# Performance work log

Hardware: AMD Instinct MI355X
Metric: run time of the kernel (lower is better)

The kernel has to match this reference:

```python
import jax, jax.numpy as jnp
import numpy as np

MIN_EXPERT_CAPACITY = 4
EPS = 1e-9
CAPACITY_FACTOR = 1.25  # training-mode capacity factor
LOSS_COEF = 0.01


def _top1(t):
    idx = jnp.argmax(t, axis=-1)
    val = jnp.take_along_axis(t, idx[..., None], axis=-1)[..., 0]
    return val, idx


def _cumsum_exclusive(t):
    # exclusive cumsum along the group (token) axis, dim=-2
    return jnp.cumsum(t, axis=-2) - t


def _top2_gating(logits, importance=None):
    """lucidrains Top2Gating, policy='all', training capacity factor.
    logits: [..., group, num_gates]. Returns (dispatch [...,g,e,c], combine, loss)."""
    group_size = logits.shape[-2]
    num_gates = logits.shape[-1]
    raw_gates = jax.nn.softmax(logits, axis=-1)

    gate_1, index_1 = _top1(raw_gates)
    mask_1 = jax.nn.one_hot(index_1, num_gates, dtype=raw_gates.dtype)
    density_1_proxy = raw_gates
    if importance is not None:
        eq_one = (importance == 1.0).astype(raw_gates.dtype)
        mask_1 = mask_1 * eq_one[..., None]
        gate_1 = gate_1 * eq_one
        density_1_proxy = density_1_proxy * eq_one[..., None]

    gate_2, index_2 = _top1(raw_gates * (1.0 - mask_1))
    mask_2 = jax.nn.one_hot(index_2, num_gates, dtype=raw_gates.dtype)
    if importance is not None:
        mask_2 = mask_2 * (importance > 0.0).astype(raw_gates.dtype)[..., None]

    denom = gate_1 + gate_2 + EPS
    gate_1 = gate_1 / denom
    gate_2 = gate_2 / denom

    density_1 = mask_1.mean(axis=-2)
    loss = jnp.mean(density_1_proxy.mean(axis=-2) * density_1) * (num_gates ** 2)

    # second_policy == 'all': keep every second-place expert
    cap = max(MIN_EXPERT_CAPACITY, min(group_size, int(group_size * CAPACITY_FACTOR / num_gates)))

    pos_1 = _cumsum_exclusive(mask_1) * mask_1
    mask_1 = mask_1 * (pos_1 < cap).astype(mask_1.dtype)
    mask_1_count = mask_1.sum(axis=-2, keepdims=True)
    mask_1_flat = mask_1.sum(axis=-1)
    pos_1 = pos_1.sum(axis=-1)
    gate_1 = gate_1 * mask_1_flat

    pos_2 = (_cumsum_exclusive(mask_2) + mask_1_count) * mask_2
    mask_2 = mask_2 * (pos_2 < cap).astype(mask_2.dtype)
    mask_2_flat = mask_2.sum(axis=-1)
    pos_2 = pos_2.sum(axis=-1)
    gate_2 = gate_2 * mask_2_flat

    combine = (
        gate_1[..., None, None] * mask_1_flat[..., None, None]
        * jax.nn.one_hot(index_1, num_gates, dtype=gate_1.dtype)[..., None]
        * jax.nn.one_hot(pos_1.astype(jnp.int32), cap, dtype=gate_1.dtype)[..., None, :]
        + gate_2[..., None, None] * mask_2_flat[..., None, None]
        * jax.nn.one_hot(index_2, num_gates, dtype=gate_2.dtype)[..., None]
        * jax.nn.one_hot(pos_2.astype(jnp.int32), cap, dtype=gate_2.dtype)[..., None, :]
    )
    dispatch = (combine != 0).astype(combine.dtype)
    return dispatch, combine, loss


def setup_inputs() -> dict:
    B, N, D, EO, EI, H = 8, 2048, 1024, 4, 4, 4096
    k = jax.random.split(jax.random.key(0), 5)
    return {
        "inputs": jax.random.normal(k[0], (B, N, D), jnp.float32),
        "w_gate_outer": jax.random.normal(k[1], (D, EO), jnp.float32) * D ** -0.5,
        "w_gate_inner": jax.random.normal(k[2], (EO, D, EI), jnp.float32) * D ** -0.5,
        "w1": jax.random.uniform(k[3], (EO, EI, D, H), jnp.float32, -(H ** -0.5), H ** -0.5),
        "w2": jax.random.uniform(k[4], (EO, EI, H, D), jnp.float32, -(D ** -0.5), D ** -0.5),
    }


def reference(inputs, w_gate_outer, w_gate_inner, w1, w2):
    # outer gating over tokens: [b,n,d] -> dispatch [b,n,eo,c_o]
    disp_o, comb_o, loss_o = _top2_gating(jnp.einsum('bnd,de->bne', inputs, w_gate_outer))
    exp_in_o = jnp.einsum('bnd,bnec->ebcd', inputs, disp_o)          # [eo,b,c_o,d]

    importance = comb_o.transpose(2, 0, 3, 1).sum(axis=-1)           # [eo,b,c_o]
    importance = 0.5 * ((importance > 0.5).astype(inputs.dtype)
                        + (importance > 0.0).astype(inputs.dtype))

    # inner gating per outer expert: [eo,b,c_o,d] -> dispatch [eo,b,c_o,ei,c_i]
    disp_i, comb_i, loss_i = _top2_gating(
        jnp.einsum('ebnd,edg->ebng', exp_in_o, w_gate_inner), importance=importance)
    exp_in = jnp.einsum('ebnd,ebnfc->efbcd', exp_in_o, disp_i)       # [eo,ei,b,c_i,d]

    # grouped-expert FFN (ReLU)
    hidden = jax.nn.relu(jnp.einsum('efbcd,efdh->efbch', exp_in, w1))
    exp_out = jnp.einsum('efbch,efhd->efbcd', hidden, w2)

    out_o = jnp.einsum('efbcd,ebnfc->ebnd', exp_out, comb_i)         # combine inner
    output = jnp.einsum('ebcd,bnec->bnd', out_o, comb_o)             # combine outer
    return output, (loss_o + loss_i) * LOSS_COEF
```

## Files before the change

kernel.cpp:

```cpp
#include <hip/hip_runtime.h>
#include <cstdint>
#include <cstddef>

#define B_    8
#define N_    2048
#define D_    1024
#define EO_   4
#define EI_   4
#define H_    4096
#define CO_   640
#define CI_   200
#define NTOK  (B_*N_)
#define NSLOT (EO_*B_*CO_)
#define MP    1664
#define NISLP (16*MP)
#define GP    4
#define EPS_  1e-9f

typedef unsigned short u16;
typedef __attribute__((ext_vector_type(8))) short bf16x8;
typedef __attribute__((ext_vector_type(4))) float f32x4;
typedef __attribute__((ext_vector_type(4))) unsigned short u16x4;

__device__ __forceinline__ void split2(float v, u16& h, u16& l) {
  unsigned b  = __float_as_uint(v);
  unsigned hb = (b + 0x7FFFu + ((b >> 16) & 1u)) >> 16;
  float fh = __uint_as_float(hb << 16);
  float r  = v - fh;
  unsigned rb = __float_as_uint(r);
  unsigned lb = (rb + 0x7FFFu + ((rb >> 16) & 1u)) >> 16;
  h = (u16)hb; l = (u16)lb;
}

__device__ __forceinline__ void gload_lds16(const void* g, void* l) {
  __builtin_amdgcn_global_load_lds((const __attribute__((address_space(1))) void*)g,
                                   (__attribute__((address_space(3))) void*)l, 16, 0, 0);
}

__global__ void k_outer_logits(const float* __restrict__ x, const float* __restrict__ wgo,
                               float* __restrict__ logits) {
  int wave = (blockIdx.x * blockDim.x + threadIdx.x) >> 6;
  int lane = threadIdx.x & 63;
  const float*  xr = x + (size_t)wave * D_;
  const float4* w4 = (const float4*)wgo;
  float a0 = 0.f, a1 = 0.f, a2 = 0.f, a3 = 0.f;
#pragma unroll
  for (int i = 0; i < 16; ++i) {
    int d = i * 64 + lane;
    float xv = xr[d];
    float4 wv = w4[d];
    a0 += xv * wv.x; a1 += xv * wv.y; a2 += xv * wv.z; a3 += xv * wv.w;
  }
#pragma unroll
  for (int o = 32; o > 0; o >>= 1) {
    a0 += __shfl_xor(a0, o, 64); a1 += __shfl_xor(a1, o, 64);
    a2 += __shfl_xor(a2, o, 64); a3 += __shfl_xor(a3, o, 64);
  }
  if (lane == 0) ((float4*)logits)[wave] = make_float4(a0, a1, a2, a3);
}

__global__ void k_outer_gate(const float* __restrict__ logits,
                             int* __restrict__ t_idx1, int* __restrict__ t_idx2,
                             int* __restrict__ t_pos1, int* __restrict__ t_pos2,
                             float* __restrict__ t_g1, float* __restrict__ t_g2,
                             int* __restrict__ oslot_tok, float* __restrict__ oslot_gate,
                             float* __restrict__ loss_acc) {
  int b = blockIdx.x;
  int lane = threadIdx.x;
  unsigned long long lmask = (1ULL << lane) - 1ULL;
  int cnt1[4] = {0, 0, 0, 0};
  float accProxy[4] = {0.f, 0.f, 0.f, 0.f};

  for (int ch = 0; ch < N_ / 64; ++ch) {
    int t = b * N_ + ch * 64 + lane;
    float4 l4 = ((const float4*)logits)[t];
    float p[4];
    {
      float m = fmaxf(fmaxf(l4.x, l4.y), fmaxf(l4.z, l4.w));
      p[0] = expf(l4.x - m); p[1] = expf(l4.y - m); p[2] = expf(l4.z - m); p[3] = expf(l4.w - m);
      float inv = 1.f / (p[0] + p[1] + p[2] + p[3]);
      p[0] *= inv; p[1] *= inv; p[2] *= inv; p[3] *= inv;
    }
    int i1 = 0; float g1 = p[0];
#pragma unroll
    for (int g = 1; g < 4; ++g) if (p[g] > g1) { g1 = p[g]; i1 = g; }
    int i2 = 0; float g2 = -1.f;
#pragma unroll
    for (int g = 0; g < 4; ++g) if (g != i1 && p[g] > g2) { g2 = p[g]; i2 = g; }
    float denom = g1 + g2 + EPS_;
    float g1n = g1 / denom, g2n = g2 / denom;
    accProxy[0] += p[0]; accProxy[1] += p[1]; accProxy[2] += p[2]; accProxy[3] += p[3];

    int pos1 = 0;
#pragma unroll
    for (int e = 0; e < 4; ++e) {
      unsigned long long mb = __ballot(i1 == e);
      if (i1 == e) pos1 = cnt1[e] + (int)__popcll(mb & lmask);
      cnt1[e] += (int)__popcll(mb);
    }
    bool kept1 = pos1 < CO_;
    t_idx1[t] = i1; t_idx2[t] = i2; t_pos1[t] = pos1;
    t_g1[t] = kept1 ? g1n : 0.f;
    t_g2[t] = g2n;
    if (kept1) {
      int s = (i1 * B_ + b) * CO_ + pos1;
      oslot_tok[s] = t; oslot_gate[s] = g1n;
    }
  }

#pragma unroll
  for (int e = 0; e < 4; ++e) {
    float v = accProxy[e];
#pragma unroll
    for (int o = 32; o > 0; o >>= 1) v += __shfl_xor(v, o, 64);
    accProxy[e] = v;
  }
  if (lane == 0) {
    float part = 0.f;
#pragma unroll
    for (int e = 0; e < 4; ++e)
      part += (accProxy[e] / (float)N_) * ((float)cnt1[e] / (float)N_);
    atomicAdd(loss_acc, part * 16.f / (float)(B_ * EO_));
  }

  int cnt2[4];
#pragma unroll
  for (int e = 0; e < 4; ++e) cnt2[e] = cnt1[e] < CO_ ? cnt1[e] : CO_;
  for (int ch = 0; ch < N_ / 64; ++ch) {
    int t = b * N_ + ch * 64 + lane;
    int i2 = t_idx2[t];
    int pos2 = 0;
#pragma unroll
    for (int e = 0; e < 4; ++e) {
      unsigned long long mb = __ballot(i2 == e);
      if (i2 == e) pos2 = cnt2[e] + (int)__popcll(mb & lmask);
      cnt2[e] += (int)__popcll(mb);
    }
    bool kept2 = pos2 < CO_;
    float g2n = t_g2[t];
    t_pos2[t] = pos2;
    t_g2[t] = kept2 ? g2n : 0.f;
    if (kept2) {
      int s = (i2 * B_ + b) * CO_ + pos2;
      oslot_tok[s] = t; oslot_gate[s] = g2n;
    }
  }
}

__global__ void k_inner_logits(const float* __restrict__ x, const float* __restrict__ wgi,
                               const int* __restrict__ oslot_tok, float* __restrict__ ilogits) {
  int wave = (blockIdx.x * blockDim.x + threadIdx.x) >> 6;
  int lane = threadIdx.x & 63;
  int e = wave / (B_ * CO_);
  int tok = oslot_tok[wave];
  float a0 = 0.f, a1 = 0.f, a2 = 0.f, a3 = 0.f;
  if (tok >= 0) {
    const float*  xr = x + (size_t)tok * D_;
    const float4* w4 = (const float4*)wgi + (size_t)e * D_;
#pragma unroll
    for (int i = 0; i < 16; ++i) {
      int d = i * 64 + lane;
      float xv = xr[d];
      float4 wv = w4[d];
      a0 += xv * wv.x; a1 += xv * wv.y; a2 += xv * wv.z; a3 += xv * wv.w;
    }
  }
#pragma unroll
  for (int o = 32; o > 0; o >>= 1) {
    a0 += __shfl_xor(a0, o, 64); a1 += __shfl_xor(a1, o, 64);
    a2 += __shfl_xor(a2, o, 64); a3 += __shfl_xor(a3, o, 64);
  }
  if (lane == 0) ((float4*)ilogits)[wave] = make_float4(a0, a1, a2, a3);
}

__global__ void k_inner_gate(const float* __restrict__ ilogits,
                             const int* __restrict__ oslot_tok, const float* __restrict__ oslot_gate,
                             int* __restrict__ os_f1, int* __restrict__ os_p1, float* __restrict__ os_g1,
                             int* __restrict__ os_f2, int* __restrict__ os_p2, float* __restrict__ os_g2,
                             int* __restrict__ islot_tok, float* __restrict__ islot_coef,
                             float* __restrict__ loss_acc) {
  int eb = blockIdx.x;
  int e = eb >> 3, b = eb & 7;
  int base = eb * CO_;
  int lane = threadIdx.x;
  unsigned long long lmask = (1ULL << lane) - 1ULL;
  int cnt1[4] = {0, 0, 0, 0};
  float accProxy[4] = {0.f, 0.f, 0.f, 0.f};

  for (int ch = 0; ch < CO_ / 64; ++ch) {
    int s = base + ch * 64 + lane;
    float go = oslot_gate[s];
    bool eq1 = (go > 0.5f);
    float4 l4 = ((const float4*)ilogits)[s];
    float p[4];
    {
      float m = fmaxf(fmaxf(l4.x, l4.y), fmaxf(l4.z, l4.w));
      p[0] = expf(l4.x - m); p[1] = expf(l4.y - m); p[2] = expf(l4.z - m); p[3] = expf(l4.w - m);
      float inv = 1.f / (p[0] + p[1] + p[2] + p[3]);
      p[0] *= inv; p[1] *= inv; p[2] *= inv; p[3] *= inv;
    }
    int i1 = 0; float g1raw = p[0];
#pragma unroll
    for (int g = 1; g < 4; ++g) if (p[g] > g1raw) { g1raw = p[g]; i1 = g; }
    int i2; float g2raw;
    if (eq1) {
      i2 = 0; g2raw = -1.f;
#pragma unroll
      for (int g = 0; g < 4; ++g) if (g != i1 && p[g] > g2raw) { g2raw = p[g]; i2 = g; }
    } else {
      i2 = i1; g2raw = g1raw;
    }
    float gate1 = eq1 ? g1raw : 0.f;
    float gate2 = g2raw;
    float denom = gate1 + gate2 + EPS_;
    float g1n = gate1 / denom, g2n = gate2 / denom;
    if (eq1) { accProxy[0] += p[0]; accProxy[1] += p[1]; accProxy[2] += p[2]; accProxy[3] += p[3]; }

    int pos1 = 0;
#pragma unroll
    for (int g = 0; g < 4; ++g) {
      bool hit = eq1 && (i1 == g);
      unsigned long long mb = __ballot(hit);
      if (hit) pos1 = cnt1[g] + (int)__popcll(mb & lmask);
      cnt1[g] += (int)__popcll(mb);
    }
    bool kept1 = eq1 && (pos1 < CI_);
    os_f1[s] = i1; os_p1[s] = pos1; os_g1[s] = kept1 ? g1n : 0.f;
    os_f2[s] = i2; os_g2[s] = g2n;
    if (kept1) {
      int ip = (e * EI_ + i1) * MP + b * CI_ + pos1;
      islot_tok[ip]  = oslot_tok[s];
      islot_coef[ip] = go * g1n;
    }
  }

#pragma unroll
  for (int g = 0; g < 4; ++g) {
    float v = accProxy[g];
#pragma unroll
    for (int o = 32; o > 0; o >>= 1) v += __shfl_xor(v, o, 64);
    accProxy[g] = v;
  }
  if (lane == 0) {
    float part = 0.f;
#pragma unroll
    for (int g = 0; g < 4; ++g)
      part += (accProxy[g] / (float)CO_) * ((float)cnt1[g] / (float)CO_);
    atomicAdd(loss_acc, part * 16.f / (float)(EO_ * B_ * EI_));
  }

  int cnt2[4];
#pragma unroll
  for (int g = 0; g < 4; ++g) cnt2[g] = cnt1[g] < CI_ ? cnt1[g] : CI_;
  for (int ch = 0; ch < CO_ / 64; ++ch) {
    int s = base + ch * 64 + lane;
    float go2 = oslot_gate[s];
    bool act2 = (go2 > 0.f);
    int i2 = os_f2[s];
    int pos2 = 0;
#pragma unroll
    for (int g = 0; g < 4; ++g) {
      bool hit = act2 && (i2 == g);
      unsigned long long mb = __ballot(hit);
      if (hit) pos2 = cnt2[g] + (int)__popcll(mb & lmask);
      cnt2[g] += (int)__popcll(mb);
    }
    bool kept2 = act2 && (pos2 < CI_);
    float g2n = os_g2[s];
    os_p2[s] = pos2;
    os_g2[s] = kept2 ? g2n : 0.f;
    if (kept2) {
      int ip = (e * EI_ + i2) * MP + b * CI_ + pos2;
      islot_tok[ip]  = oslot_tok[s];
      islot_coef[ip] = go2 * g2n;
    }
  }
}

__global__ __launch_bounds__(256) void k_gather_a(const float* __restrict__ x,
                                                  const int* __restrict__ itok,
                                                  u16* __restrict__ Ah, u16* __restrict__ Al) {
  int ls = blockIdx.x;
  int tok = itok[ls];
  int t = threadIdx.x;
  float4 v = make_float4(0.f, 0.f, 0.f, 0.f);
  if (tok >= 0) v = ((const float4*)(x + (size_t)tok * D_))[t];
  u16 h0, l0, h1, l1, h2, l2, h3, l3;
  split2(v.x, h0, l0); split2(v.y, h1, l1); split2(v.z, h2, l2); split2(v.w, h3, l3);
  u16x4 hv = {h0, h1, h2, h3};
  u16x4 lv = {l0, l1, l2, l3};
  *(u16x4*)(Ah + (size_t)ls * D_ + t * 4) = hv;
  *(u16x4*)(Al + (size_t)ls * D_ + t * 4) = lv;
}

__global__ __launch_bounds__(256) void k_conv_w(const float* __restrict__ w,
                                                u16* __restrict__ wh, u16* __restrict__ wl,
                                                int K, int N) {
  __shared__ float tile[32][33];
  int pair = blockIdx.z;
  int n0 = blockIdx.x * 32, k0 = blockIdx.y * 32;
  const float* wp = w + (size_t)pair * K * N;
  int tx = threadIdx.x & 31, ty = threadIdx.x >> 5;
#pragma unroll
  for (int i = 0; i < 4; ++i) {
    int r = ty + i * 8;
    tile[r][tx] = wp[(size_t)(k0 + r) * N + n0 + tx];
  }
  __syncthreads();
  size_t obase = (size_t)pair * N * K;
#pragma unroll
  for (int i = 0; i < 4; ++i) {
    int r = ty + i * 8;
    u16 h, l; split2(tile[tx][r], h, l);
    size_t o = obase + (size_t)(n0 + r) * K + k0 + tx;
    wh[o] = h; wl[o] = l;
  }
}

template<int KK>
__device__ __forceinline__ void gemm_core(const u16* __restrict__ Ah, const u16* __restrict__ Al,
                                          size_t arow0,
                                          const u16* __restrict__ Bh, const u16* __restrict__ Bl,
                                          size_t brow0,
                                          short* lds, f32x4 (&acc)[4][4]) {
  const int tid  = threadIdx.x;
  const int lane = tid & 63;
  const int w    = tid >> 6;
  const int wm   = w >> 1, wn = w & 1;
  short* LAh = lds;
  short* LAl = lds + 4096;
  short* LBh = lds + 8192;
  short* LBl = lds + 12288;
  const int sr = lane & 15, sk = lane >> 4;
  const size_t aoff0 = (arow0 + (size_t)(2 * w) * 16 + sr) * KK + sk * 8;
  const size_t aoff1 = aoff0 + (size_t)16 * KK;
  const size_t boff0 = (brow0 + (size_t)(2 * w) * 16 + sr) * KK + sk * 8;
  const size_t boff1 = boff0 + (size_t)16 * KK;
  short* dAh0 = LAh + (2 * w) * 512; short* dAh1 = dAh0 + 512;
  short* dAl0 = LAl + (2 * w) * 512; short* dAl1 = dAl0 + 512;
  short* dBh0 = LBh + (2 * w) * 512; short* dBh1 = dBh0 + 512;
  short* dBl0 = LBl + (2 * w) * 512; short* dBl1 = dBl0 + 512;

  for (int k0 = 0; k0 < KK; k0 += 32) {
    gload_lds16(Ah + aoff0 + k0, dAh0);
    gload_lds16(Ah + aoff1 + k0, dAh1);
    gload_lds16(Al + aoff0 + k0, dAl0);
    gload_lds16(Al + aoff1 + k0, dAl1);
    gload_lds16(Bh + boff0 + k0, dBh0);
    gload_lds16(Bh + boff1 + k0, dBh1);
    gload_lds16(Bl + boff0 + k0, dBl0);
    gload_lds16(Bl + boff1 + k0, dBl1);
    __syncthreads();
    bf16x8 ahf[4], alf[4], bhf[4], blf[4];
#pragma unroll
    for (int f = 0; f < 4; ++f) {
      ahf[f] = *(const bf16x8*)(LAh + (wm * 4 + f) * 512 + lane * 8);
      alf[f] = *(const bf16x8*)(LAl + (wm * 4 + f) * 512 + lane * 8);
      bhf[f] = *(const bf16x8*)(LBh + (wn * 4 + f) * 512 + lane * 8);
      blf[f] = *(const bf16x8*)(LBl + (wn * 4 + f) * 512 + lane * 8);
    }
#pragma unroll
    for (int mf = 0; mf < 4; ++mf)
#pragma unroll
      for (int nf = 0; nf < 4; ++nf) {
        acc[mf][nf] = __builtin_amdgcn_mfma_f32_16x16x32_bf16(ahf[mf], bhf[nf], acc[mf][nf], 0, 0, 0);
        acc[mf][nf] = __builtin_amdgcn_mfma_f32_16x16x32_bf16(ahf[mf], blf[nf], acc[mf][nf], 0, 0, 0);
        acc[mf][nf] = __builtin_amdgcn_mfma_f32_16x16x32_bf16(alf[mf], bhf[nf], acc[mf][nf], 0, 0, 0);
      }
    __syncthreads();
  }
}

__global__ __launch_bounds__(256) void k_gemm1(const u16* __restrict__ Ah, const u16* __restrict__ Al,
                                               const u16* __restrict__ Wh, const u16* __restrict__ Wl,
                                               u16* __restrict__ hh, u16* __restrict__ hl) {
  __shared__ short lds[16384];
  f32x4 acc[4][4];
  const f32x4 z4 = {0.f, 0.f, 0.f, 0.f};
#pragma unroll
  for (int i = 0; i < 4; ++i)
#pragma unroll
    for (int j = 0; j < 4; ++j) acc[i][j] = z4;
  const int zb = blockIdx.z;
  const size_t arow0 = (size_t)zb * MP + blockIdx.x * 128;
  const size_t brow0 = (size_t)zb * H_ + blockIdx.y * 128;
  gemm_core<D_>(Ah, Al, arow0, Wh, Wl, brow0, lds, acc);

  const int lane = threadIdx.x & 63, w = threadIdx.x >> 6;
  const int wm = w >> 1, wn = w & 1;
  const int cl = lane & 15, rh = lane >> 4;
  const size_t row_base = (size_t)zb * MP + blockIdx.x * 128 + wm * 64;
  const int col0 = blockIdx.y * 128 + wn * 64;
#pragma unroll
  for (int mf = 0; mf < 4; ++mf)
#pragma unroll
    for (int j = 0; j < 4; ++j) {
      size_t r = row_base + mf * 16 + rh * 4 + j;
      size_t base = r * H_ + col0;
#pragma unroll
      for (int nf = 0; nf < 4; ++nf) {
        float v = fmaxf(acc[mf][nf][j], 0.f);
        u16 h, l; split2(v, h, l);
        hh[base + nf * 16 + cl] = h;
        hl[base + nf * 16 + cl] = l;
      }
    }
}

__global__ __launch_bounds__(256) void k_gemm2(const u16* __restrict__ Hh, const u16* __restrict__ Hl,
                                               const u16* __restrict__ Wh, const u16* __restrict__ Wl,
                                               const int* __restrict__ itok, const float* __restrict__ icoef,
                                               float* __restrict__ out) {
  __shared__ short lds[16384];
  f32x4 acc[4][4];
  const f32x4 z4 = {0.f, 0.f, 0.f, 0.f};
#pragma unroll
  for (int i = 0; i < 4; ++i)
#pragma unroll
    for (int j = 0; j < 4; ++j) acc[i][j] = z4;
  const int zb = blockIdx.z;
  const size_t arow0 = (size_t)zb * MP + blockIdx.x * 128;
  const size_t brow0 = (size_t)zb * D_ + blockIdx.y * 128;
  gemm_core<H_>(Hh, Hl, arow0, Wh, Wl, brow0, lds, acc);

  const int lane = threadIdx.x & 63, w = threadIdx.x >> 6;
  const int wm = w >> 1, wn = w & 1;
  const int cl = lane & 15, rh = lane >> 4;
  const int row0 = blockIdx.x * 128 + wm * 64;
  const int col0 = blockIdx.y * 128 + wn * 64;
#pragma unroll
  for (int mf = 0; mf < 4; ++mf)
#pragma unroll
    for (int j = 0; j < 4; ++j) {
      int r = row0 + mf * 16 + rh * 4 + j;
      int sp = zb * MP + r;
      int tok = itok[sp];
      if (tok < 0) continue;
      float cf = icoef[sp];
      float* ob = out + (size_t)tok * D_ + col0;
#pragma unroll
      for (int nf = 0; nf < 4; ++nf)
        atomicAdd(ob + nf * 16 + cl, cf * acc[mf][nf][j]);
    }
}

__global__ void k_loss(const float* __restrict__ loss_acc, float* __restrict__ out_loss) {
  if (threadIdx.x == 0 && blockIdx.x == 0) out_loss[0] = loss_acc[0] * 0.01f;
}

extern "C" void kernel_launch(void* const* d_in, const int* in_sizes, int n_in,
                              void* d_out, int out_size, void* d_ws, size_t ws_size,
                              hipStream_t stream) {
  const float* x   = (const float*)d_in[0];
  const float* wgo = (const float*)d_in[1];
  const float* wgi = (const float*)d_in[2];
  const float* w1  = (const float*)d_in[3];
  const float* w2  = (const float*)d_in[4];
  float* out = (float*)d_out;

  char* ws = (char*)d_ws;
  size_t off = 0;
  auto alloc = [&](size_t bytes) -> void* {
    void* p = ws + off;
    off = (off + bytes + 255) & ~(size_t)255;
    return p;
  };
  float* logits_o   = (float*)alloc((size_t)NTOK * 4 * sizeof(float));
  float* ilogits    = (float*)alloc((size_t)NSLOT * 4 * sizeof(float));
  int*   t_idx1     = (int*)alloc((size_t)NTOK * sizeof(int));
  int*   t_idx2     = (int*)alloc((size_t)NTOK * sizeof(int));
  int*   t_pos1     = (int*)alloc((size_t)NTOK * sizeof(int));
  int*   t_pos2     = (int*)alloc((size_t)NTOK * sizeof(int));
  float* t_g1       = (float*)alloc((size_t)NTOK * sizeof(float));
  float* t_g2       = (float*)alloc((size_t)NTOK * sizeof(float));
  int*   oslot_tok  = (int*)alloc((size_t)NSLOT * sizeof(int));
  float* oslot_gate = (float*)alloc((size_t)NSLOT * sizeof(float));
  int*   os_f1      = (int*)alloc((size_t)NSLOT * sizeof(int));
  int*   os_p1      = (int*)alloc((size_t)NSLOT * sizeof(int));
  float* os_g1      = (float*)alloc((size_t)NSLOT * sizeof(float));
  int*   os_f2      = (int*)alloc((size_t)NSLOT * sizeof(int));
  int*   os_p2      = (int*)alloc((size_t)NSLOT * sizeof(int));
  float* os_g2      = (float*)alloc((size_t)NSLOT * sizeof(float));
  int*   islot_tok  = (int*)alloc((size_t)NISLP * sizeof(int));
  float* islot_coef = (float*)alloc((size_t)NISLP * sizeof(float));
  float* loss_acc   = (float*)alloc(256);
  u16* Ah = (u16*)alloc((size_t)GP * MP * D_ * sizeof(u16));
  u16* Al = (u16*)alloc((size_t)GP * MP * D_ * sizeof(u16));
  u16* Wh = (u16*)alloc((size_t)GP * H_ * D_ * sizeof(u16));
  u16* Wl = (u16*)alloc((size_t)GP * H_ * D_ * sizeof(u16));
  u16* hh = (u16*)alloc((size_t)GP * MP * H_ * sizeof(u16));
  u16* hl = (u16*)alloc((size_t)GP * MP * H_ * sizeof(u16));

  hipMemsetAsync(oslot_tok, 0xFF, (size_t)NSLOT * sizeof(int), stream);
  hipMemsetAsync(oslot_gate, 0, (size_t)NSLOT * sizeof(float), stream);
  hipMemsetAsync(islot_tok, 0xFF, (size_t)NISLP * sizeof(int), stream);
  hipMemsetAsync(islot_coef, 0, (size_t)NISLP * sizeof(float), stream);
  hipMemsetAsync(loss_acc, 0, sizeof(float), stream);
  hipMemsetAsync(out, 0, (size_t)NTOK * D_ * sizeof(float), stream);

  k_outer_logits<<<NTOK / 4, 256, 0, stream>>>(x, wgo, logits_o);
  k_outer_gate<<<B_, 64, 0, stream>>>(logits_o, t_idx1, t_idx2, t_pos1, t_pos2,
                                      t_g1, t_g2, oslot_tok, oslot_gate, loss_acc);
  k_inner_logits<<<NSLOT / 4, 256, 0, stream>>>(x, wgi, oslot_tok, ilogits);
  k_inner_gate<<<EO_ * B_, 64, 0, stream>>>(ilogits, oslot_tok, oslot_gate,
                                            os_f1, os_p1, os_g1, os_f2, os_p2, os_g2,
                                            islot_tok, islot_coef, loss_acc);
  for (int g = 0; g < 4; ++g) {
    int pair0 = g * GP;
    k_gather_a<<<GP * MP, 256, 0, stream>>>(x, islot_tok + (size_t)pair0 * MP, Ah, Al);
    k_conv_w<<<dim3(H_ / 32, D_ / 32, GP), 256, 0, stream>>>(
        w1 + (size_t)pair0 * D_ * H_, Wh, Wl, D_, H_);
    k_gemm1<<<dim3(13, H_ / 128, GP), 256, 0, stream>>>(Ah, Al, Wh, Wl, hh, hl);
    k_conv_w<<<dim3(D_ / 32, H_ / 32, GP), 256, 0, stream>>>(
        w2 + (size_t)pair0 * H_ * D_, Wh, Wl, H_, D_);
    k_gemm2<<<dim3(13, D_ / 128, GP), 256, 0, stream>>>(
        hh, hl, Wh, Wl, islot_tok + (size_t)pair0 * MP, islot_coef + (size_t)pair0 * MP, out);
  }
  k_loss<<<1, 64, 0, stream>>>(loss_acc, out + (size_t)NTOK * D_);
}
```

Measured before the change: 3.130 ms.

## Split-K second expert GEMM and remap GEMM blocks across XCDs for L2 reuse

The second FFN GEMM is split four ways along its K dimension of 4096, which quadruples its grid and relies on the existing atomicAdd epilogue to sum the partial results. Both GEMM kernels now remap the linear block id so that blocks sharing an expert pair and weight columns land on the same XCD, aiming at better L2 reuse of A and W tiles. The original gemm2 grid had only 416 blocks, too few to fill the GPU with long K loops. The cost is four times as many fp32 atomic adds into the output, plus a hard-coded block mapping that assumes 8 XCDs and these exact grid sizes.

```diff
diff --git a/kernel.cpp b/kernel.cpp
--- a/kernel.cpp
+++ b/kernel.cpp
@@ -317,11 +317,11 @@
   }
 }
 
-template<int KK>
+template<int LDK>
 __device__ __forceinline__ void gemm_core(const u16* __restrict__ Ah, const u16* __restrict__ Al,
                                           size_t arow0,
                                           const u16* __restrict__ Bh, const u16* __restrict__ Bl,
-                                          size_t brow0,
+                                          size_t brow0, int kbeg, int kend,
                                           short* lds, f32x4 (&acc)[4][4]) {
   const int tid  = threadIdx.x;
   const int lane = tid & 63;
@@ -332,16 +332,16 @@
   short* LBh = lds + 8192;
   short* LBl = lds + 12288;
   const int sr = lane & 15, sk = lane >> 4;
-  const size_t aoff0 = (arow0 + (size_t)(2 * w) * 16 + sr) * KK + sk * 8;
-  const size_t aoff1 = aoff0 + (size_t)16 * KK;
-  const size_t boff0 = (brow0 + (size_t)(2 * w) * 16 + sr) * KK + sk * 8;
-  const size_t boff1 = boff0 + (size_t)16 * KK;
+  const size_t aoff0 = (arow0 + (size_t)(2 * w) * 16 + sr) * LDK + sk * 8;
+  const size_t aoff1 = aoff0 + (size_t)16 * LDK;
+  const size_t boff0 = (brow0 + (size_t)(2 * w) * 16 + sr) * LDK + sk * 8;
+  const size_t boff1 = boff0 + (size_t)16 * LDK;
   short* dAh0 = LAh + (2 * w) * 512; short* dAh1 = dAh0 + 512;
   short* dAl0 = LAl + (2 * w) * 512; short* dAl1 = dAl0 + 512;
   short* dBh0 = LBh + (2 * w) * 512; short* dBh1 = dBh0 + 512;
   short* dBl0 = LBl + (2 * w) * 512; short* dBl1 = dBl0 + 512;
 
-  for (int k0 = 0; k0 < KK; k0 += 32) {
+  for (int k0 = kbeg; k0 < kend; k0 += 32) {
     gload_lds16(Ah + aoff0 + k0, dAh0);
     gload_lds16(Ah + aoff1 + k0, dAh1);
     gload_lds16(Al + aoff0 + k0, dAl0);
@@ -375,22 +375,29 @@
                                                const u16* __restrict__ Wh, const u16* __restrict__ Wl,
                                                u16* __restrict__ hh, u16* __restrict__ hl) {
   __shared__ short lds[16384];
+  int lin = blockIdx.x + 13 * (blockIdx.y + 32 * blockIdx.z);
+  int xcd = lin & 7, slot = lin >> 3;
+  int g   = (xcd << 1) | (slot >= 104 ? 1 : 0);
+  int idx = slot >= 104 ? slot - 104 : slot;
+  int bx  = idx % 13;
+  int by  = (g & 3) * 8 + idx / 13;
+  int zb  = g >> 2;
+
   f32x4 acc[4][4];
   const f32x4 z4 = {0.f, 0.f, 0.f, 0.f};
 #pragma unroll
   for (int i = 0; i < 4; ++i)
 #pragma unroll
     for (int j = 0; j < 4; ++j) acc[i][j] = z4;
-  const int zb = blockIdx.z;
-  const size_t arow0 = (size_t)zb * MP + blockIdx.x * 128;
-  const size_t brow0 = (size_t)zb * H_ + blockIdx.y * 128;
-  gemm_core<D_>(Ah, Al, arow0, Wh, Wl, brow0, lds, acc);
+  const size_t arow0 = (size_t)zb * MP + bx * 128;
+  const size_t brow0 = (size_t)zb * H_ + by * 128;
+  gemm_core<D_>(Ah, Al, arow0, Wh, Wl, brow0, 0, D_, lds, acc);
 
   const int lane = threadIdx.x & 63, w = threadIdx.x >> 6;
   const int wm = w >> 1, wn = w & 1;
   const int cl = lane & 15, rh = lane >> 4;
-  const size_t row_base = (size_t)zb * MP + blockIdx.x * 128 + wm * 64;
-  const int col0 = blockIdx.y * 128 + wn * 64;
+  const size_t row_base = (size_t)zb * MP + bx * 128 + wm * 64;
+  const int col0 = by * 128 + wn * 64;
 #pragma unroll
   for (int mf = 0; mf < 4; ++mf)
 #pragma unroll
@@ -412,22 +419,30 @@
                                                const int* __restrict__ itok, const float* __restrict__ icoef,
                                                float* __restrict__ out) {
   __shared__ short lds[16384];
+  int lin = blockIdx.x + 13 * (blockIdx.y + 8 * blockIdx.z);
+  int xcd = lin & 7, slot = lin >> 3;
+  int g   = (xcd << 1) | (slot >= 104 ? 1 : 0);
+  int idx = slot >= 104 ? slot - 104 : slot;
+  int bx  = idx % 13;
+  int by  = idx / 13;
+  int zb  = g >> 2;
+  int kc  = g & 3;
+
   f32x4 acc[4][4];
   const f32x4 z4 = {0.f, 0.f, 0.f, 0.f};
 #pragma unroll
   for (int i = 0; i < 4; ++i)
 #pragma unroll
     for (int j = 0; j < 4; ++j) acc[i][j] = z4;
-  const int zb = blockIdx.z;
-  const size_t arow0 = (size_t)zb * MP + blockIdx.x * 128;
-  const size_t brow0 = (size_t)zb * D_ + blockIdx.y * 128;
-  gemm_core<H_>(Hh, Hl, arow0, Wh, Wl, brow0, lds, acc);
+  const size_t arow0 = (size_t)zb * MP + bx * 128;
+  const size_t brow0 = (size_t)zb * D_ + by * 128;
+  gemm_core<H_>(Hh, Hl, arow0, Wh, Wl, brow0, kc * 1024, kc * 1024 + 1024, lds, acc);
 
   const int lane = threadIdx.x & 63, w = threadIdx.x >> 6;
   const int wm = w >> 1, wn = w & 1;
   const int cl = lane & 15, rh = lane >> 4;
-  const int row0 = blockIdx.x * 128 + wm * 64;
-  const int col0 = blockIdx.y * 128 + wn * 64;
+  const int row0 = bx * 128 + wm * 64;
+  const int col0 = by * 128 + wn * 64;
 #pragma unroll
   for (int mf = 0; mf < 4; ++mf)
 #pragma unroll
@@ -513,7 +528,7 @@
     k_gemm1<<<dim3(13, H_ / 128, GP), 256, 0, stream>>>(Ah, Al, Wh, Wl, hh, hl);
     k_conv_w<<<dim3(D_ / 32, H_ / 32, GP), 256, 0, stream>>>(
         w2 + (size_t)pair0 * H_ * D_, Wh, Wl, H_, D_);
-    k_gemm2<<<dim3(13, D_ / 128, GP), 256, 0, stream>>>(
+    k_gemm2<<<dim3(13, 8, 16), 256, 0, stream>>>(
         hh, hl, Wh, Wl, islot_tok + (size_t)pair0 * MP, islot_coef + (size_t)pair0 * MP, out);
   }
   k_loss<<<1, 64, 0, stream>>>(loss_acc, out + (size_t)NTOK * D_);
```

Result: faster. 3.007 ms (-3.9%).
